# Kernel optimization log

Hardware: AMD Instinct MI355X
Metric: run time of the kernel (lower is better)

Reference implementation:

```python
import jax, jax.numpy as jnp
import numpy as np
from jax import lax

C = 16
FIRE_RATE = 0.5
STEP_SIZE = 1.0


def _fixed_kernel():
    _i = np.array([0, 1, 0], dtype=np.float32)
    I = np.outer(_i, _i)
    dx = (np.outer([1, 2, 1], [-1, 0, 1]) / 8.0).astype(np.float32)
    dy = dx.T
    lap = np.array([[0.25, 0.5, 0.25], [0.5, -3, 0.5], [0.25, 0.5, 0.25]], dtype=np.float32)
    av = np.ones((3, 3), dtype=np.float32) / 9.0
    k = np.stack([I, dx, dy, lap, av], -1)            # [3,3,5]
    k = np.tile(k, (1, 1, C))                          # [3,3,5*C], channel-major blocks of 5
    return jnp.asarray(k[:, :, None, :])               # HWIO [3,3,1,5*C]

KERNEL = _fixed_kernel()


def setup_inputs() -> dict:
    key = jax.random.key(0)
    ks = jax.random.split(key, 5)
    B, S = 4, 512
    x = jax.random.normal(ks[0], (B, S, S, C), jnp.float32)
    noise = jax.random.normal(ks[1], (B, S, S, 1), jnp.float32)
    W1 = jax.random.normal(ks[2], (5 * C, 4 * C), jnp.float32) * (1.0 / np.sqrt(5 * C))
    b1 = jnp.zeros((4 * C,), jnp.float32)
    W2 = jax.random.normal(ks[3], (4 * C, 2 * C), jnp.float32) * (1.0 / np.sqrt(4 * C))
    b2 = jnp.zeros((2 * C,), jnp.float32)
    W3 = jax.random.normal(ks[4], (2 * C, C), jnp.float32) * (1.0 / np.sqrt(2 * C))
    b3 = jnp.zeros((C,), jnp.float32)
    return {"x": x, "noise": noise, "W1": W1, "b1": b1, "W2": W2, "b2": b2, "W3": W3, "b3": b3}


def _swish(z):
    return z * jax.nn.sigmoid(z)


def reference(x, noise, W1, b1, W2, b2, W3, b3):
    # perceive: depthwise 3x3 conv with 5 fixed kernels per channel -> [B,H,W,5*C]
    y = lax.conv_general_dilated(
        x, KERNEL, window_strides=(1, 1), padding="SAME",
        dimension_numbers=("NHWC", "HWIO", "NHWC"), feature_group_count=C)
    # 3-layer 1x1 conv MLP
    h = _swish(jnp.einsum("bhwc,cd->bhwd", y, W1) + b1)
    h = _swish(jnp.einsum("bhwc,cd->bhwd", h, W2) + b2)
    dx = (jnp.einsum("bhwc,cd->bhwd", h, W3) + b3) * STEP_SIZE
    # stochastic update mask: normal noise <= fire_rate
    update_mask = (noise <= FIRE_RATE).astype(jnp.float32)  # [B,H,W,1]
    return x + dx * update_mask
```

## Files before the change

### kernel.cpp

```cpp
#include <hip/hip_runtime.h>

typedef __bf16 bf16x8 __attribute__((ext_vector_type(8)));
typedef float f32x4 __attribute__((ext_vector_type(4)));
typedef float f32x16 __attribute__((ext_vector_type(16)));
typedef short short8 __attribute__((ext_vector_type(8)));

#define S 512
#define CH 16

#define ELT(v, c) ((c)==0 ? (v).x : (c)==1 ? (v).y : (c)==2 ? (v).z : (v).w)

__device__ __forceinline__ float swishf(float z) {
    return z * __builtin_amdgcn_rcpf(1.0f + __expf(-z));
}

__global__ void prep_weights(const float* __restrict__ W1, const float* __restrict__ b1,
                             const float* __restrict__ W2, const float* __restrict__ b2,
                             const float* __restrict__ W3, const float* __restrict__ b3,
                             short* __restrict__ wsf, float* __restrict__ wsb)
{
    int idx = blockIdx.x * 256 + threadIdx.x;
    if (idx < 8192) {
        int fi = idx >> 9, rem = idx & 511;
        int lane = rem >> 3, j = rem & 7;
        int col = lane & 31, hi = lane >> 5;
        int jp = (j & 3) + 8 * (j >> 2);
        float v;
        if (fi < 10) {
            int n = fi / 5, s = fi - n * 5;
            int rowW = hi * 40 + s * 8 + j;
            v = W1[rowW * 64 + n * 32 + col];
        } else if (fi < 14) {
            int t = fi - 10;
            int rowW = (t >> 1) * 32 + 4 * hi + (t & 1) * 16 + jp;
            v = W2[rowW * 32 + col];
        } else {
            int t = fi - 14;
            int rowW = 4 * hi + t * 16 + jp;
            v = (col < 16) ? W3[rowW * 16 + col] : 0.0f;
        }
        __bf16 b = (__bf16)v;
        wsf[idx] = __builtin_bit_cast(short, b);
    }
    if (blockIdx.x == 0) {
        int t = threadIdx.x;
        if (t < 64) wsb[t] = b1[t];
        else if (t < 96) wsb[t] = b2[t - 64];
        else if (t < 112) wsb[t] = b3[t - 96];
    }
}

__global__ __launch_bounds__(256, 5) void nca_fused(
    const float* __restrict__ x, const float* __restrict__ noise,
    const short* __restrict__ wsf, const float* __restrict__ wsb,
    float* __restrict__ out)
{
    __shared__ short wlds[8192];
    {
        const int4* src = reinterpret_cast<const int4*>(wsf);
        int4* dst = reinterpret_cast<int4*>(wlds);
        for (int i = threadIdx.x; i < 1024; i += 256) dst[i] = src[i];
    }
    __syncthreads();

    const int tid = threadIdx.x;
    const int bid = blockIdx.x;
    const int st = bid & 15;
    const int rg = (bid >> 4) & 127;
    const int bb = bid >> 11;
    const int wv = tid >> 6, lane = tid & 63;
    const int col = lane & 31, hi = lane >> 5;
    const int row = rg * 4 + wv;
    const int px0 = st * 32;

    short8 af[5];
    {
        const bool rv0 = row > 0, rv2 = row < S - 1;
        const bool colInt = (px0 != 0) && (px0 != 480);
        const float* xb = x + (size_t)bb * S * S * CH;
        const int p = col;
#pragma unroll
        for (int qi = 0; qi < 2; ++qi) {
            const int q = hi * 2 + qi;
            float4 A[3][3];
#pragma unroll
            for (int rr = 0; rr < 3; ++rr) {
                bool rok = (rr == 0) ? rv0 : (rr == 2 ? rv2 : true);
                if (rok) {
                    const float* rp = xb + (size_t)(row - 1 + rr) * S * CH + q * 4;
                    if (colInt) {
                        const float* bp = rp + (px0 + p - 1) * CH;
                        A[rr][0] = *reinterpret_cast<const float4*>(bp);
                        A[rr][1] = *reinterpret_cast<const float4*>(bp + CH);
                        A[rr][2] = *reinterpret_cast<const float4*>(bp + 2 * CH);
                    } else {
#pragma unroll
                        for (int d = 0; d < 3; ++d) {
                            int c = px0 + p - 1 + d;
                            int cl = min(max(c, 0), S - 1);
                            float4 v = *reinterpret_cast<const float4*>(rp + cl * CH);
                            if ((unsigned)c >= (unsigned)S) v = make_float4(0.f, 0.f, 0.f, 0.f);
                            A[rr][d] = v;
                        }
                    }
                } else {
                    A[rr][0] = make_float4(0.f, 0.f, 0.f, 0.f);
                    A[rr][1] = A[rr][0]; A[rr][2] = A[rr][0];
                }
            }
#pragma unroll
            for (int cc = 0; cc < 4; ++cc) {
                float a00 = ELT(A[0][0], cc), a01 = ELT(A[0][1], cc), a02 = ELT(A[0][2], cc);
                float a10 = ELT(A[1][0], cc), a11 = ELT(A[1][1], cc), a12 = ELT(A[1][2], cc);
                float a20 = ELT(A[2][0], cc), a21 = ELT(A[2][1], cc), a22 = ELT(A[2][2], cc);
                float cw0 = a00 + 2.f * a10 + a20;
                float cw1 = a01 + 2.f * a11 + a21;
                float cw2 = a02 + 2.f * a12 + a22;
                float rw0 = a00 + 2.f * a01 + a02;
                float rw2 = a20 + 2.f * a21 + a22;
                float fI  = a11;
                float fdx = (cw2 - cw0) * 0.125f;
                float fdy = (rw2 - rw0) * 0.125f;
                float flp = 0.25f * (cw0 + 2.f * cw1 + cw2) - 4.f * a11;
                float fav = ((cw0 + cw1 + cw2) - (a10 + a11 + a12)) * (1.f / 9.f);
                const int mb = (qi * 4 + cc) * 5;
                af[(mb + 0) >> 3][(mb + 0) & 7] = __builtin_bit_cast(short, (__bf16)fI);
                af[(mb + 1) >> 3][(mb + 1) & 7] = __builtin_bit_cast(short, (__bf16)fdx);
                af[(mb + 2) >> 3][(mb + 2) & 7] = __builtin_bit_cast(short, (__bf16)fdy);
                af[(mb + 3) >> 3][(mb + 3) & 7] = __builtin_bit_cast(short, (__bf16)flp);
                af[(mb + 4) >> 3][(mb + 4) & 7] = __builtin_bit_cast(short, (__bf16)fav);
            }
        }
    }

    const short8* wf = reinterpret_cast<const short8*>(wlds);

    f32x16 acc1[2];
#pragma unroll
    for (int n = 0; n < 2; ++n) {
        f32x16 acc = {};
#pragma unroll
        for (int s = 0; s < 5; ++s) {
            bf16x8 a = __builtin_bit_cast(bf16x8, wf[(n * 5 + s) * 64 + lane]);
            bf16x8 b = __builtin_bit_cast(bf16x8, af[s]);
            acc = __builtin_amdgcn_mfma_f32_32x32x16_bf16(a, b, acc, 0, 0, 0);
        }
        acc1[n] = acc;
    }

    short8 b2f[4];
#pragma unroll
    for (int t = 0; t < 4; ++t) {
        int n = t >> 1;
        float4 bq0 = *reinterpret_cast<const float4*>(wsb + n * 32 + 4 * hi + 16 * (t & 1));
        float4 bq1 = *reinterpret_cast<const float4*>(wsb + n * 32 + 4 * hi + 16 * (t & 1) + 8);
#pragma unroll
        for (int j = 0; j < 8; ++j) {
            float bias = (j < 4) ? ELT(bq0, j & 3) : ELT(bq1, j & 3);
            float h = swishf(acc1[n][(t & 1) * 8 + j] + bias);
            b2f[t][j] = __builtin_bit_cast(short, (__bf16)h);
        }
    }

    f32x16 acc2 = {};
#pragma unroll
    for (int t = 0; t < 4; ++t) {
        bf16x8 a = __builtin_bit_cast(bf16x8, wf[(10 + t) * 64 + lane]);
        acc2 = __builtin_amdgcn_mfma_f32_32x32x16_bf16(a, __builtin_bit_cast(bf16x8, b2f[t]), acc2, 0, 0, 0);
    }

    short8 b3f[2];
#pragma unroll
    for (int t = 0; t < 2; ++t) {
        float4 cq0 = *reinterpret_cast<const float4*>(wsb + 64 + 4 * hi + 16 * t);
        float4 cq1 = *reinterpret_cast<const float4*>(wsb + 64 + 4 * hi + 16 * t + 8);
#pragma unroll
        for (int j = 0; j < 8; ++j) {
            float bias = (j < 4) ? ELT(cq0, j & 3) : ELT(cq1, j & 3);
            float h = swishf(acc2[t * 8 + j] + bias);
            b3f[t][j] = __builtin_bit_cast(short, (__bf16)h);
        }
    }

    f32x16 acc3 = {};
#pragma unroll
    for (int t = 0; t < 2; ++t) {
        bf16x8 a = __builtin_bit_cast(bf16x8, wf[(14 + t) * 64 + lane]);
        acc3 = __builtin_amdgcn_mfma_f32_32x32x16_bf16(a, __builtin_bit_cast(bf16x8, b3f[t]), acc3, 0, 0, 0);
    }

    size_t pix = ((size_t)(bb * S + row)) * S + px0 + col;
    float msk = (noise[pix] <= 0.5f) ? 1.f : 0.f;
    float4 bA = *reinterpret_cast<const float4*>(wsb + 96 + 4 * hi);
    float4 bB = *reinterpret_cast<const float4*>(wsb + 96 + 8 + 4 * hi);
    const float* xp = x + pix * CH;
    float4 c0 = *reinterpret_cast<const float4*>(xp + 4 * hi);
    float4 c1 = *reinterpret_cast<const float4*>(xp + 8 + 4 * hi);
    float4 o0, o1;
    o0.x = c0.x + (acc3[0] + bA.x) * msk;
    o0.y = c0.y + (acc3[1] + bA.y) * msk;
    o0.z = c0.z + (acc3[2] + bA.z) * msk;
    o0.w = c0.w + (acc3[3] + bA.w) * msk;
    o1.x = c1.x + (acc3[4] + bB.x) * msk;
    o1.y = c1.y + (acc3[5] + bB.y) * msk;
    o1.z = c1.z + (acc3[6] + bB.z) * msk;
    o1.w = c1.w + (acc3[7] + bB.w) * msk;
    *reinterpret_cast<float4*>(out + pix * CH + 4 * hi) = o0;
    *reinterpret_cast<float4*>(out + pix * CH + 8 + 4 * hi) = o1;
}

extern "C" void kernel_launch(void* const* d_in, const int* in_sizes, int n_in,
                              void* d_out, int out_size, void* d_ws, size_t ws_size,
                              hipStream_t stream)
{
    const float* x     = (const float*)d_in[0];
    const float* noise = (const float*)d_in[1];
    const float* W1    = (const float*)d_in[2];
    const float* b1    = (const float*)d_in[3];
    const float* W2    = (const float*)d_in[4];
    const float* b2    = (const float*)d_in[5];
    const float* W3    = (const float*)d_in[6];
    const float* b3    = (const float*)d_in[7];
    short* wsf = (short*)d_ws;
    float* wsb = (float*)((char*)d_ws + 16384);
    float* out = (float*)d_out;

    hipLaunchKernelGGL(prep_weights, dim3(32), dim3(256), 0, stream,
                       W1, b1, W2, b2, W3, b3, wsf, wsb);
    hipLaunchKernelGGL(nca_fused, dim3(4 * 128 * 16), dim3(256), 0, stream,
                       x, noise, wsf, wsb, out);
}
```

Measured before the change: 177.7 us.

## Fold fixed perception stencil into W1 and feed raw 3x3 neighborhood to MFMA

Precomputes combined weights that merge the fixed depthwise 3x3 perception filters with W1, so the first layer becomes a GEMM over the raw 3x3x16 neighborhood (K=144) instead of over 80 computed features. This removes the per-pixel scalar stencil arithmetic from the VALU and replaces it with more MFMA work and bf16 packing of the raw inputs. The trade-off is 18 instead of 10 first-layer MFMAs, a larger LDS weight table, and lower occupancy (launch bounds 5 to 4). Accuracy may also shift slightly because inputs are rounded to bf16 before filtering.

```diff
diff --git a/kernel.cpp b/kernel.cpp
--- a/kernel.cpp
+++ b/kernel.cpp
@@ -1,7 +1,6 @@
 #include <hip/hip_runtime.h>
 
 typedef __bf16 bf16x8 __attribute__((ext_vector_type(8)));
-typedef float f32x4 __attribute__((ext_vector_type(4)));
 typedef float f32x16 __attribute__((ext_vector_type(16)));
 typedef short short8 __attribute__((ext_vector_type(8)));
 
@@ -20,22 +19,34 @@
                              short* __restrict__ wsf, float* __restrict__ wsb)
 {
     int idx = blockIdx.x * 256 + threadIdx.x;
-    if (idx < 8192) {
+    if (idx < 12288) {
         int fi = idx >> 9, rem = idx & 511;
         int lane = rem >> 3, j = rem & 7;
         int col = lane & 31, hi = lane >> 5;
         int jp = (j & 3) + 8 * (j >> 2);
         float v;
-        if (fi < 10) {
-            int n = fi / 5, s = fi - n * 5;
-            int rowW = hi * 40 + s * 8 + j;
-            v = W1[rowW * 64 + n * 32 + col];
-        } else if (fi < 14) {
-            int t = fi - 10;
+        if (fi < 18) {
+            int n = fi / 9, s = fi - n * 9;
+            int dr = s / 3, dc = s - dr * 3;
+            int c = hi * 8 + j;
+            const float wgt0 = (dr == 1) ? 2.f : 1.f;
+            const float wgt1 = (dc == 1) ? 2.f : 1.f;
+            const float dlt0 = (float)(dr - 1);
+            const float dlt1 = (float)(dc - 1);
+            const float lapm[9] = {0.25f, 0.5f, 0.25f, 0.5f, -3.f, 0.5f, 0.25f, 0.5f, 0.25f};
+            float kI  = (s == 4) ? 1.f : 0.f;
+            float kdx = wgt0 * dlt1 * 0.125f;
+            float kdy = dlt0 * wgt1 * 0.125f;
+            float klp = lapm[s];
+            float kav = 1.f / 9.f;
+            const float* wr = W1 + (c * 5) * 64 + n * 32 + col;
+            v = kI * wr[0] + kdx * wr[64] + kdy * wr[128] + klp * wr[192] + kav * wr[256];
+        } else if (fi < 22) {
+            int t = fi - 18;
             int rowW = (t >> 1) * 32 + 4 * hi + (t & 1) * 16 + jp;
             v = W2[rowW * 32 + col];
         } else {
-            int t = fi - 14;
+            int t = fi - 22;
             int rowW = 4 * hi + t * 16 + jp;
             v = (col < 16) ? W3[rowW * 16 + col] : 0.0f;
         }
@@ -50,16 +61,16 @@
     }
 }
 
-__global__ __launch_bounds__(256, 5) void nca_fused(
+__global__ __launch_bounds__(256, 4) void nca_fused(
     const float* __restrict__ x, const float* __restrict__ noise,
     const short* __restrict__ wsf, const float* __restrict__ wsb,
     float* __restrict__ out)
 {
-    __shared__ short wlds[8192];
+    __shared__ short wlds[12288];
     {
         const int4* src = reinterpret_cast<const int4*>(wsf);
         int4* dst = reinterpret_cast<int4*>(wlds);
-        for (int i = threadIdx.x; i < 1024; i += 256) dst[i] = src[i];
+        for (int i = threadIdx.x; i < 1536; i += 256) dst[i] = src[i];
     }
     __syncthreads();
 
@@ -73,62 +84,57 @@
     const int row = rg * 4 + wv;
     const int px0 = st * 32;
 
-    short8 af[5];
+    short8 bfr[9];
     {
-        const bool rv0 = row > 0, rv2 = row < S - 1;
+        const float* xb = x + (size_t)bb * S * S * CH + hi * 8;
+        const bool rowInt = (row > 0) && (row < S - 1);
         const bool colInt = (px0 != 0) && (px0 != 480);
-        const float* xb = x + (size_t)bb * S * S * CH;
-        const int p = col;
-#pragma unroll
-        for (int qi = 0; qi < 2; ++qi) {
-            const int q = hi * 2 + qi;
-            float4 A[3][3];
-#pragma unroll
-            for (int rr = 0; rr < 3; ++rr) {
-                bool rok = (rr == 0) ? rv0 : (rr == 2 ? rv2 : true);
-                if (rok) {
-                    const float* rp = xb + (size_t)(row - 1 + rr) * S * CH + q * 4;
-                    if (colInt) {
-                        const float* bp = rp + (px0 + p - 1) * CH;
-                        A[rr][0] = *reinterpret_cast<const float4*>(bp);
-                        A[rr][1] = *reinterpret_cast<const float4*>(bp + CH);
-                        A[rr][2] = *reinterpret_cast<const float4*>(bp + 2 * CH);
-                    } else {
-#pragma unroll
-                        for (int d = 0; d < 3; ++d) {
-                            int c = px0 + p - 1 + d;
-                            int cl = min(max(c, 0), S - 1);
-                            float4 v = *reinterpret_cast<const float4*>(rp + cl * CH);
-                            if ((unsigned)c >= (unsigned)S) v = make_float4(0.f, 0.f, 0.f, 0.f);
-                            A[rr][d] = v;
-                        }
-                    }
-                } else {
-                    A[rr][0] = make_float4(0.f, 0.f, 0.f, 0.f);
-                    A[rr][1] = A[rr][0]; A[rr][2] = A[rr][0];
+        if (rowInt && colInt) {
+#pragma unroll
+            for (int dr = 0; dr < 3; ++dr) {
+                const float* rp = xb + ((size_t)(row - 1 + dr) * S + (px0 + col - 1)) * CH;
+#pragma unroll
+                for (int dc = 0; dc < 3; ++dc) {
+                    float4 v0 = *reinterpret_cast<const float4*>(rp + dc * CH);
+                    float4 v1 = *reinterpret_cast<const float4*>(rp + dc * CH + 4);
+                    short8 f;
+                    f[0] = __builtin_bit_cast(short, (__bf16)v0.x);
+                    f[1] = __builtin_bit_cast(short, (__bf16)v0.y);
+                    f[2] = __builtin_bit_cast(short, (__bf16)v0.z);
+                    f[3] = __builtin_bit_cast(short, (__bf16)v0.w);
+                    f[4] = __builtin_bit_cast(short, (__bf16)v1.x);
+                    f[5] = __builtin_bit_cast(short, (__bf16)v1.y);
+                    f[6] = __builtin_bit_cast(short, (__bf16)v1.z);
+                    f[7] = __builtin_bit_cast(short, (__bf16)v1.w);
+                    bfr[dr * 3 + dc] = f;
                 }
             }
-#pragma unroll
-            for (int cc = 0; cc < 4; ++cc) {
-                float a00 = ELT(A[0][0], cc), a01 = ELT(A[0][1], cc), a02 = ELT(A[0][2], cc);
-                float a10 = ELT(A[1][0], cc), a11 = ELT(A[1][1], cc), a12 = ELT(A[1][2], cc);
-                float a20 = ELT(A[2][0], cc), a21 = ELT(A[2][1], cc), a22 = ELT(A[2][2], cc);
-                float cw0 = a00 + 2.f * a10 + a20;
-                float cw1 = a01 + 2.f * a11 + a21;
-                float cw2 = a02 + 2.f * a12 + a22;
-                float rw0 = a00 + 2.f * a01 + a02;
-                float rw2 = a20 + 2.f * a21 + a22;
-                float fI  = a11;
-                float fdx = (cw2 - cw0) * 0.125f;
-                float fdy = (rw2 - rw0) * 0.125f;
-                float flp = 0.25f * (cw0 + 2.f * cw1 + cw2) - 4.f * a11;
-                float fav = ((cw0 + cw1 + cw2) - (a10 + a11 + a12)) * (1.f / 9.f);
-                const int mb = (qi * 4 + cc) * 5;
-                af[(mb + 0) >> 3][(mb + 0) & 7] = __builtin_bit_cast(short, (__bf16)fI);
-                af[(mb + 1) >> 3][(mb + 1) & 7] = __builtin_bit_cast(short, (__bf16)fdx);
-                af[(mb + 2) >> 3][(mb + 2) & 7] = __builtin_bit_cast(short, (__bf16)fdy);
-                af[(mb + 3) >> 3][(mb + 3) & 7] = __builtin_bit_cast(short, (__bf16)flp);
-                af[(mb + 4) >> 3][(mb + 4) & 7] = __builtin_bit_cast(short, (__bf16)fav);
+        } else {
+#pragma unroll
+            for (int dr = 0; dr < 3; ++dr) {
+                int gr = row - 1 + dr;
+                bool rok = (unsigned)gr < (unsigned)S;
+                int grc = min(max(gr, 0), S - 1);
+#pragma unroll
+                for (int dc = 0; dc < 3; ++dc) {
+                    int c = px0 + col - 1 + dc;
+                    bool ok = rok && ((unsigned)c < (unsigned)S);
+                    int cl = min(max(c, 0), S - 1);
+                    const float* p = xb + ((size_t)grc * S + cl) * CH;
+                    float4 v0 = *reinterpret_cast<const float4*>(p);
+                    float4 v1 = *reinterpret_cast<const float4*>(p + 4);
+                    if (!ok) { v0 = make_float4(0.f,0.f,0.f,0.f); v1 = v0; }
+                    short8 f;
+                    f[0] = __builtin_bit_cast(short, (__bf16)v0.x);
+                    f[1] = __builtin_bit_cast(short, (__bf16)v0.y);
+                    f[2] = __builtin_bit_cast(short, (__bf16)v0.z);
+                    f[3] = __builtin_bit_cast(short, (__bf16)v0.w);
+                    f[4] = __builtin_bit_cast(short, (__bf16)v1.x);
+                    f[5] = __builtin_bit_cast(short, (__bf16)v1.y);
+                    f[6] = __builtin_bit_cast(short, (__bf16)v1.z);
+                    f[7] = __builtin_bit_cast(short, (__bf16)v1.w);
+                    bfr[dr * 3 + dc] = f;
+                }
             }
         }
     }
@@ -140,10 +146,9 @@
     for (int n = 0; n < 2; ++n) {
         f32x16 acc = {};
 #pragma unroll
-        for (int s = 0; s < 5; ++s) {
-            bf16x8 a = __builtin_bit_cast(bf16x8, wf[(n * 5 + s) * 64 + lane]);
-            bf16x8 b = __builtin_bit_cast(bf16x8, af[s]);
-            acc = __builtin_amdgcn_mfma_f32_32x32x16_bf16(a, b, acc, 0, 0, 0);
+        for (int s = 0; s < 9; ++s) {
+            bf16x8 a = __builtin_bit_cast(bf16x8, wf[(n * 9 + s) * 64 + lane]);
+            acc = __builtin_amdgcn_mfma_f32_32x32x16_bf16(a, __builtin_bit_cast(bf16x8, bfr[s]), acc, 0, 0, 0);
         }
         acc1[n] = acc;
     }
@@ -165,7 +170,7 @@
     f32x16 acc2 = {};
 #pragma unroll
     for (int t = 0; t < 4; ++t) {
-        bf16x8 a = __builtin_bit_cast(bf16x8, wf[(10 + t) * 64 + lane]);
+        bf16x8 a = __builtin_bit_cast(bf16x8, wf[(18 + t) * 64 + lane]);
         acc2 = __builtin_amdgcn_mfma_f32_32x32x16_bf16(a, __builtin_bit_cast(bf16x8, b2f[t]), acc2, 0, 0, 0);
     }
 
@@ -185,7 +190,7 @@
     f32x16 acc3 = {};
 #pragma unroll
     for (int t = 0; t < 2; ++t) {
-        bf16x8 a = __builtin_bit_cast(bf16x8, wf[(14 + t) * 64 + lane]);
+        bf16x8 a = __builtin_bit_cast(bf16x8, wf[(22 + t) * 64 + lane]);
         acc3 = __builtin_amdgcn_mfma_f32_32x32x16_bf16(a, __builtin_bit_cast(bf16x8, b3f[t]), acc3, 0, 0, 0);
     }
 
@@ -222,10 +227,10 @@
     const float* W3    = (const float*)d_in[6];
     const float* b3    = (const float*)d_in[7];
     short* wsf = (short*)d_ws;
-    float* wsb = (float*)((char*)d_ws + 16384);
+    float* wsb = (float*)((char*)d_ws + 24576);
     float* out = (float*)d_out;
 
-    hipLaunchKernelGGL(prep_weights, dim3(32), dim3(256), 0, stream,
+    hipLaunchKernelGGL(prep_weights, dim3(48), dim3(256), 0, stream,
                        W1, b1, W2, b2, W3, b3, wsf, wsb);
     hipLaunchKernelGGL(nca_fused, dim3(4 * 128 * 16), dim3(256), 0, stream,
                        x, noise, wsf, wsb, out);
```

Result: no change. 180.1 us (+1.3%).
